# Performance work log

Hardware: AMD Instinct MI355X
Metric: run time of the kernel (lower is better)

Reference implementation:

```python
import jax, jax.numpy as jnp
import numpy as np

B, S, H, E, TOP_K = 4, 2048, 1024, 16, 4


def setup_inputs() -> dict:
    key = jax.random.key(0)
    ks = jax.random.split(key, 12)
    sc = 1.0 / np.sqrt(H)
    inp = {
        "x": jax.random.normal(ks[0], (B, S, H), dtype=jnp.float32),
        "image": jax.random.normal(ks[1], (B, S, H), dtype=jnp.float32),
        "text": jax.random.normal(ks[2], (B, S, H), dtype=jnp.float32),
        "audio": jax.random.normal(ks[3], (B, S, H), dtype=jnp.float32),
        # generalized router linear
        "Wg": jax.random.uniform(ks[4], (H, E), jnp.float32, -sc, sc),
        "bg": jax.random.uniform(ks[5], (E,), jnp.float32, -sc, sc),
        # per-modality router linears
        "Wi": jax.random.uniform(ks[6], (H, E), jnp.float32, -sc, sc),
        "bi": jax.random.uniform(ks[7], (E,), jnp.float32, -sc, sc),
        "Wt": jax.random.uniform(ks[8], (H, E), jnp.float32, -sc, sc),
        "bt": jax.random.uniform(ks[9], (E,), jnp.float32, -sc, sc),
        "Wa": jax.random.uniform(ks[10], (H, E), jnp.float32, -sc, sc),
        "ba": jax.random.uniform(ks[11], (E,), jnp.float32, -sc, sc),
    }
    return inp


def reference(x, image, text, audio, Wg, bg, Wi, bi, Wt, bt, Wa, ba):
    # combined_logits = generalized_router(x) + sum_m modality_router_m(modality_m)
    logits = (
        jnp.einsum("bsh,he->bse", x, Wg) + bg
        + jnp.einsum("bsh,he->bse", image, Wi) + bi
        + jnp.einsum("bsh,he->bse", text, Wt) + bt
        + jnp.einsum("bsh,he->bse", audio, Wa) + ba
    )  # [B,S,E]
    router_probs = jax.nn.softmax(logits, axis=-1)
    top_k_probs, top_k_indices = jax.lax.top_k(router_probs, TOP_K)
    top_k_probs = top_k_probs / jnp.sum(top_k_probs, axis=-1, keepdims=True)
    prob_per_expert = jnp.mean(router_probs, axis=(0, 1))  # [E]
    aux_loss = jnp.sum(prob_per_expert * jnp.log(prob_per_expert * E + 1e-9))
    return (top_k_indices, top_k_probs, aux_loss)
```

## Files before the change

kernel.cpp:

```cpp
#include <hip/hip_runtime.h>
#include <math.h>

constexpr int kTokens = 8192;
constexpr int kH      = 1024;
constexpr int kE      = 16;
constexpr int kTopK   = 4;
constexpr int kNC     = 16;

__global__ __launch_bounds__(256, 5)
void router_fmac(const float* __restrict__ x,   const float* __restrict__ img,
                 const float* __restrict__ txt, const float* __restrict__ aud,
                 const float* __restrict__ Wg,  const float* __restrict__ Wi,
                 const float* __restrict__ Wt,  const float* __restrict__ Wa,
                 float* __restrict__ partials)
{
    __shared__ float smem[5120];

    const int t  = threadIdx.x;
    const int w  = __builtin_amdgcn_readfirstlane(t >> 6);
    const int ln = t & 63;
    const int hs    = blockIdx.x & 15;
    const int tg    = blockIdx.x >> 4;
    const int tok0  = tg * 64;
    const int hbase = hs * 64;

    const float* Xs[4] = { x,  img, txt, aud };
    const float* Ws[4] = { Wg, Wi,  Wt,  Wa  };

    const int sc = t & 7;
    const int sr = t >> 3;

    {
        const float* src = Xs[0] + (size_t)tok0 * kH + hbase + sc * 4;
        const float4 va = *(const float4*)(src + (size_t)sr * kH);
        const float4 vb = *(const float4*)(src + (size_t)(sr + 32) * kH);
        *(float4*)&smem[sr * 36 + sc * 4] = va;
        *(float4*)&smem[(sr + 32) * 36 + sc * 4] = vb;
    }
    __syncthreads();

    double dacc[kE];
#pragma unroll
    for (int e = 0; e < kE; ++e) dacc[e] = 0.0;
    float facc[kE];

#pragma unroll
    for (int p = 0; p < 8; ++p) {
        const int m = p >> 1;
        const int s = p & 1;

        float4 na, nb;
        if (p < 7) {
            const int m2 = (p + 1) >> 1, s2 = (p + 1) & 1;
            const float* src = Xs[m2] + (size_t)tok0 * kH + hbase + s2 * 32 + sc * 4;
            na = *(const float4*)(src + (size_t)sr * kH);
            nb = *(const float4*)(src + (size_t)(sr + 32) * kH);
        }

        if (s == 0) {
#pragma unroll
            for (int e = 0; e < kE; ++e) facc[e] = 0.f;
        }

        const float* buf   = smem + (p & 1) * 2304;
        const float* wbase = Ws[m] + (size_t)(hbase + s * 32 + w * 8) * kE;

#pragma unroll
        for (int k4 = 0; k4 < 2; ++k4) {
            const float4 xv = *(const float4*)&buf[ln * 36 + w * 8 + k4 * 4];
#pragma unroll
            for (int j = 0; j < 4; ++j) {
                const float xh = (j == 0) ? xv.x : (j == 1) ? xv.y : (j == 2) ? xv.z : xv.w;
                const float* wr = wbase + (k4 * 4 + j) * kE;
                const float4 w0 = *(const float4*)(wr + 0);
                const float4 w1 = *(const float4*)(wr + 4);
                const float4 w2 = *(const float4*)(wr + 8);
                const float4 w3 = *(const float4*)(wr + 12);
                facc[0]  += xh * w0.x;  facc[1]  += xh * w0.y;
                facc[2]  += xh * w0.z;  facc[3]  += xh * w0.w;
                facc[4]  += xh * w1.x;  facc[5]  += xh * w1.y;
                facc[6]  += xh * w1.z;  facc[7]  += xh * w1.w;
                facc[8]  += xh * w2.x;  facc[9]  += xh * w2.y;
                facc[10] += xh * w2.z;  facc[11] += xh * w2.w;
                facc[12] += xh * w3.x;  facc[13] += xh * w3.y;
                facc[14] += xh * w3.z;  facc[15] += xh * w3.w;
            }
        }

        if (s == 1) {
#pragma unroll
            for (int e = 0; e < kE; ++e) dacc[e] += (double)facc[e];
        }

        if (p < 7) {
            float* nbuf = smem + ((p + 1) & 1) * 2304;
            *(float4*)&nbuf[sr * 36 + sc * 4] = na;
            *(float4*)&nbuf[(sr + 32) * 36 + sc * 4] = nb;
        }
        __syncthreads();
    }

#pragma unroll
    for (int q = 0; q < 4; ++q) {
        *(float4*)&smem[(w * 64 + ln) * 20 + q * 4] =
            make_float4((float)dacc[q * 4 + 0], (float)dacc[q * 4 + 1],
                        (float)dacc[q * 4 + 2], (float)dacc[q * 4 + 3]);
    }
    __syncthreads();
    {
        const int tok = t >> 2;
        const int eq  = t & 3;
        double s0 = 0.0, s1 = 0.0, s2 = 0.0, s3 = 0.0;
#pragma unroll
        for (int ww = 0; ww < 4; ++ww) {
            const float4 v = *(const float4*)&smem[(ww * 64 + tok) * 20 + eq * 4];
            s0 += (double)v.x;  s1 += (double)v.y;
            s2 += (double)v.z;  s3 += (double)v.w;
        }
        *(float4*)&partials[((size_t)hs * kTokens + tok0 + tok) * kE + eq * 4] =
            make_float4((float)s0, (float)s1, (float)s2, (float)s3);
    }
}

__global__ __launch_bounds__(256)
void router_topk(const float* __restrict__ partials,
                 const float* __restrict__ bg, const float* __restrict__ bi,
                 const float* __restrict__ bt, const float* __restrict__ ba,
                 float* __restrict__ out, float* __restrict__ blocksum)
{
    __shared__ double lgs[64][kE + 1];
    __shared__ float  pr[64][kE + 1];

    const int t    = threadIdx.x;
    const int tq   = t >> 2;
    const int eq   = t & 3;
    const int tok0 = blockIdx.x * 64;

    double a0 = (double)bg[eq*4+0] + (double)bi[eq*4+0] + (double)bt[eq*4+0] + (double)ba[eq*4+0];
    double a1 = (double)bg[eq*4+1] + (double)bi[eq*4+1] + (double)bt[eq*4+1] + (double)ba[eq*4+1];
    double a2 = (double)bg[eq*4+2] + (double)bi[eq*4+2] + (double)bt[eq*4+2] + (double)ba[eq*4+2];
    double a3 = (double)bg[eq*4+3] + (double)bi[eq*4+3] + (double)bt[eq*4+3] + (double)ba[eq*4+3];

#pragma unroll
    for (int c = 0; c < kNC; ++c) {
        const float4 v = *(const float4*)(partials + ((size_t)c * kTokens + tok0 + tq) * kE + eq * 4);
        a0 += (double)v.x;  a1 += (double)v.y;  a2 += (double)v.z;  a3 += (double)v.w;
    }
    lgs[tq][eq*4+0] = a0;  lgs[tq][eq*4+1] = a1;
    lgs[tq][eq*4+2] = a2;  lgs[tq][eq*4+3] = a3;
    __syncthreads();

    if (t < 64) {
        const int tok = tok0 + t;
        double lg[kE];
#pragma unroll
        for (int e = 0; e < kE; ++e) lg[e] = lgs[t][e];

        double mx = lg[0];
#pragma unroll
        for (int e = 1; e < kE; ++e) mx = fmax(mx, lg[e]);

        float p[kE];
        float sum = 0.f;
#pragma unroll
        for (int e = 0; e < kE; ++e) {
            p[e] = expf((float)(lg[e] - mx));
            sum += p[e];
        }
        const float inv = 1.f / sum;
#pragma unroll
        for (int e = 0; e < kE; ++e) { p[e] *= inv; pr[t][e] = p[e]; }

        unsigned used = 0;
        float tp[kTopK];
        int   ti[kTopK];
        float s4 = 0.f;
#pragma unroll
        for (int k = 0; k < kTopK; ++k) {
            float best = -1.f;
            int   bidx = 0;
#pragma unroll
            for (int e = 0; e < kE; ++e) {
                if (!((used >> e) & 1u) && p[e] > best) { best = p[e]; bidx = e; }
            }
            used |= 1u << bidx;
            tp[k] = best;
            ti[k] = bidx;
            s4 += best;
        }
        const float rn = 1.f / s4;

        *(float4*)&out[(size_t)tok * kTopK] =
            make_float4((float)ti[0], (float)ti[1], (float)ti[2], (float)ti[3]);
        *(float4*)&out[(size_t)kTokens * kTopK + (size_t)tok * kTopK] =
            make_float4(tp[0] * rn, tp[1] * rn, tp[2] * rn, tp[3] * rn);
    }
    __syncthreads();

    if (t < kE) {
        float s = 0.f;
#pragma unroll
        for (int tk = 0; tk < 64; ++tk) s += pr[tk][t];
        blocksum[blockIdx.x * kE + t] = s;
    }
}

__global__ __launch_bounds__(64)
void router_aux(const float* __restrict__ blocksum, float* __restrict__ out)
{
    __shared__ double ps[kE];
    const int t = threadIdx.x;
    if (t < kE) {
        double s = 0.0;
        for (int b = 0; b < 128; ++b) s += (double)blocksum[b * kE + t];
        ps[t] = s / (double)kTokens;
    }
    __syncthreads();
    if (t == 0) {
        double aux = 0.0;
#pragma unroll
        for (int e = 0; e < kE; ++e) aux += ps[e] * log(ps[e] * (double)kE + 1e-9);
        out[(size_t)kTokens * kTopK * 2] = (float)aux;
    }
}

extern "C" void kernel_launch(void* const* d_in, const int* in_sizes, int n_in,
                              void* d_out, int out_size, void* d_ws, size_t ws_size,
                              hipStream_t stream)
{
    const float* x   = (const float*)d_in[0];
    const float* img = (const float*)d_in[1];
    const float* txt = (const float*)d_in[2];
    const float* aud = (const float*)d_in[3];
    const float* Wg  = (const float*)d_in[4];
    const float* bg  = (const float*)d_in[5];
    const float* Wi  = (const float*)d_in[6];
    const float* bi  = (const float*)d_in[7];
    const float* Wt  = (const float*)d_in[8];
    const float* bt  = (const float*)d_in[9];
    const float* Wa  = (const float*)d_in[10];
    const float* ba  = (const float*)d_in[11];

    float* out      = (float*)d_out;
    float* partials = (float*)d_ws;
    float* blocksum = (float*)((char*)d_ws + (size_t)kNC * kTokens * kE * 4);

    router_fmac<<<2048, 256, 0, stream>>>(x, img, txt, aud, Wg, Wi, Wt, Wa, partials);
    router_topk<<<128, 256, 0, stream>>>(partials, bg, bi, bt, ba, out, blocksum);
    router_aux<<<1, 64, 0, stream>>>(blocksum, out);
}
```

Before: 181.9 us.

## Widen H slice per block to 128 and halve split-K partials; parallelize aux reduction

The GEMV kernel now gives each block a 128-wide H slice instead of 64, so each wave processes 16 H columns per stage. This halves the number of split-K partial buffers (16 to 8), cutting partial-sum writes and reads in the top-k kernel, and halves the block count. Each stage now loads four float4 rows per thread with a 68-float padded LDS row. The aux reduction is also spread over 128 threads. The trade-off is more LDS per block, occupancy lowered from 5 to 4 blocks, and fewer blocks to hide memory latency.

```diff
diff --git a/kernel.cpp b/kernel.cpp
--- a/kernel.cpp
+++ b/kernel.cpp
@@ -5,73 +5,78 @@
 constexpr int kH      = 1024;
 constexpr int kE      = 16;
 constexpr int kTopK   = 4;
-constexpr int kNC     = 16;
-
-__global__ __launch_bounds__(256, 5)
+constexpr int kNC     = 8;
+
+__global__ __launch_bounds__(256, 4)
 void router_fmac(const float* __restrict__ x,   const float* __restrict__ img,
                  const float* __restrict__ txt, const float* __restrict__ aud,
                  const float* __restrict__ Wg,  const float* __restrict__ Wi,
                  const float* __restrict__ Wt,  const float* __restrict__ Wa,
                  float* __restrict__ partials)
 {
-    __shared__ float smem[5120];
+    __shared__ float smem[2 * 64 * 68];
 
     const int t  = threadIdx.x;
     const int w  = __builtin_amdgcn_readfirstlane(t >> 6);
     const int ln = t & 63;
-    const int hs    = blockIdx.x & 15;
-    const int tg    = blockIdx.x >> 4;
+    const int hs    = blockIdx.x & 7;
+    const int tg    = blockIdx.x >> 3;
     const int tok0  = tg * 64;
-    const int hbase = hs * 64;
+    const int hbase = hs * 128;
 
     const float* Xs[4] = { x,  img, txt, aud };
     const float* Ws[4] = { Wg, Wi,  Wt,  Wa  };
 
-    const int sc = t & 7;
-    const int sr = t >> 3;
+    const int sc = t & 15;
+    const int sr = t >> 4;
 
     {
-        const float* src = Xs[0] + (size_t)tok0 * kH + hbase + sc * 4;
-        const float4 va = *(const float4*)(src + (size_t)sr * kH);
-        const float4 vb = *(const float4*)(src + (size_t)(sr + 32) * kH);
-        *(float4*)&smem[sr * 36 + sc * 4] = va;
-        *(float4*)&smem[(sr + 32) * 36 + sc * 4] = vb;
+        const float* src = Xs[0] + (size_t)(tok0 + sr) * kH + hbase + sc * 4;
+        const float4 v0 = *(const float4*)(src);
+        const float4 v1 = *(const float4*)(src + (size_t)16 * kH);
+        const float4 v2 = *(const float4*)(src + (size_t)32 * kH);
+        const float4 v3 = *(const float4*)(src + (size_t)48 * kH);
+        float* d = smem + sr * 68 + sc * 4;
+        *(float4*)(d)           = v0;
+        *(float4*)(d + 16 * 68) = v1;
+        *(float4*)(d + 32 * 68) = v2;
+        *(float4*)(d + 48 * 68) = v3;
     }
     __syncthreads();
 
     double dacc[kE];
 #pragma unroll
     for (int e = 0; e < kE; ++e) dacc[e] = 0.0;
-    float facc[kE];
 
 #pragma unroll
     for (int p = 0; p < 8; ++p) {
         const int m = p >> 1;
         const int s = p & 1;
 
-        float4 na, nb;
+        float4 n0, n1, n2, n3;
         if (p < 7) {
             const int m2 = (p + 1) >> 1, s2 = (p + 1) & 1;
-            const float* src = Xs[m2] + (size_t)tok0 * kH + hbase + s2 * 32 + sc * 4;
-            na = *(const float4*)(src + (size_t)sr * kH);
-            nb = *(const float4*)(src + (size_t)(sr + 32) * kH);
-        }
-
-        if (s == 0) {
-#pragma unroll
-            for (int e = 0; e < kE; ++e) facc[e] = 0.f;
-        }
-
-        const float* buf   = smem + (p & 1) * 2304;
-        const float* wbase = Ws[m] + (size_t)(hbase + s * 32 + w * 8) * kE;
-
-#pragma unroll
-        for (int k4 = 0; k4 < 2; ++k4) {
-            const float4 xv = *(const float4*)&buf[ln * 36 + w * 8 + k4 * 4];
+            const float* src = Xs[m2] + (size_t)(tok0 + sr) * kH + hbase + s2 * 64 + sc * 4;
+            n0 = *(const float4*)(src);
+            n1 = *(const float4*)(src + (size_t)16 * kH);
+            n2 = *(const float4*)(src + (size_t)32 * kH);
+            n3 = *(const float4*)(src + (size_t)48 * kH);
+        }
+
+        float facc[kE];
+#pragma unroll
+        for (int e = 0; e < kE; ++e) facc[e] = 0.f;
+
+        const float* buf = smem + (p & 1) * 4352 + ln * 68 + w * 16;
+        const float* wb  = Ws[m] + (size_t)(hbase + s * 64 + w * 16) * kE;
+
+#pragma unroll
+        for (int k4 = 0; k4 < 4; ++k4) {
+            const float4 xv = *(const float4*)(buf + k4 * 4);
 #pragma unroll
             for (int j = 0; j < 4; ++j) {
                 const float xh = (j == 0) ? xv.x : (j == 1) ? xv.y : (j == 2) ? xv.z : xv.w;
-                const float* wr = wbase + (k4 * 4 + j) * kE;
+                const float* wr = wb + (k4 * 4 + j) * kE;
                 const float4 w0 = *(const float4*)(wr + 0);
                 const float4 w1 = *(const float4*)(wr + 4);
                 const float4 w2 = *(const float4*)(wr + 8);
@@ -87,15 +92,15 @@
             }
         }
 
-        if (s == 1) {
-#pragma unroll
-            for (int e = 0; e < kE; ++e) dacc[e] += (double)facc[e];
-        }
+#pragma unroll
+        for (int e = 0; e < kE; ++e) dacc[e] += (double)facc[e];
 
         if (p < 7) {
-            float* nbuf = smem + ((p + 1) & 1) * 2304;
-            *(float4*)&nbuf[sr * 36 + sc * 4] = na;
-            *(float4*)&nbuf[(sr + 32) * 36 + sc * 4] = nb;
+            float* nbuf = smem + ((p + 1) & 1) * 4352 + sr * 68 + sc * 4;
+            *(float4*)(nbuf)           = n0;
+            *(float4*)(nbuf + 16 * 68) = n1;
+            *(float4*)(nbuf + 32 * 68) = n2;
+            *(float4*)(nbuf + 48 * 68) = n3;
         }
         __syncthreads();
     }
@@ -205,21 +210,33 @@
     }
 }
 
-__global__ __launch_bounds__(64)
+__global__ __launch_bounds__(256)
 void router_aux(const float* __restrict__ blocksum, float* __restrict__ out)
 {
-    __shared__ double ps[kE];
+    __shared__ double ps[8][kE];
+    __shared__ double fin[kE];
     const int t = threadIdx.x;
+    if (t < 128) {
+        const int e  = t & 15;
+        const int bq = t >> 4;
+        double s = 0.0;
+#pragma unroll
+        for (int k = 0; k < 16; ++k)
+            s += (double)blocksum[(bq * 16 + k) * kE + e];
+        ps[bq][e] = s;
+    }
+    __syncthreads();
     if (t < kE) {
         double s = 0.0;
-        for (int b = 0; b < 128; ++b) s += (double)blocksum[b * kE + t];
-        ps[t] = s / (double)kTokens;
+#pragma unroll
+        for (int q = 0; q < 8; ++q) s += ps[q][t];
+        fin[t] = s / (double)kTokens;
     }
     __syncthreads();
     if (t == 0) {
         double aux = 0.0;
 #pragma unroll
-        for (int e = 0; e < kE; ++e) aux += ps[e] * log(ps[e] * (double)kE + 1e-9);
+        for (int e = 0; e < kE; ++e) aux += fin[e] * log(fin[e] * (double)kE + 1e-9);
         out[(size_t)kTokens * kTopK * 2] = (float)aux;
     }
 }
@@ -245,7 +262,7 @@
     float* partials = (float*)d_ws;
     float* blocksum = (float*)((char*)d_ws + (size_t)kNC * kTokens * kE * 4);
 
-    router_fmac<<<2048, 256, 0, stream>>>(x, img, txt, aud, Wg, Wi, Wt, Wa, partials);
+    router_fmac<<<1024, 256, 0, stream>>>(x, img, txt, aud, Wg, Wi, Wt, Wa, partials);
     router_topk<<<128, 256, 0, stream>>>(partials, bg, bi, bt, ba, out, blocksum);
-    router_aux<<<1, 64, 0, stream>>>(blocksum, out);
-}
+    router_aux<<<1, 256, 0, stream>>>(blocksum, out);
+}
```

Result: slower. 194.0 us (+6.7%).

## Use per-wave private LDS buffers in router GEMM and widen top-k/aux parallelism

Applied to the files above, without the earlier changes.

The main kernel now stages into wave-private LDS tiles: each wave loads exactly the H columns it consumes. Block-wide __syncthreads in the 8-phase loop become s_waitcnt plus a scheduling barrier, which also shrinks the LDS footprint. The top-k kernel moves to 32 tokens per block over twice as many blocks, with the 16 partial chunks split across thread pairs. The aux kernel reduces block sums with 256 threads. This removes block barriers and spreads the tail work, but it relies on the lgkmcnt wait alone to order LDS accesses within a wave. The aux kernel now reads 256 block sums, matching the doubled top-k grid.

```diff
diff --git a/kernel.cpp b/kernel.cpp
--- a/kernel.cpp
+++ b/kernel.cpp
@@ -14,7 +14,7 @@
                  const float* __restrict__ Wt,  const float* __restrict__ Wa,
                  float* __restrict__ partials)
 {
-    __shared__ float smem[5120];
+    __shared__ float smem[2 * 4 * 64 * 12];
 
     const int t  = threadIdx.x;
     const int w  = __builtin_amdgcn_readfirstlane(t >> 6);
@@ -27,17 +27,21 @@
     const float* Xs[4] = { x,  img, txt, aud };
     const float* Ws[4] = { Wg, Wi,  Wt,  Wa  };
 
-    const int sc = t & 7;
-    const int sr = t >> 3;
+    const int c2 = ln & 1;
+    const int rA = ln >> 1;
+
+    float* wbuf0 = smem + w * 768;
+    float* wbuf1 = smem + 3072 + w * 768;
 
     {
-        const float* src = Xs[0] + (size_t)tok0 * kH + hbase + sc * 4;
-        const float4 va = *(const float4*)(src + (size_t)sr * kH);
-        const float4 vb = *(const float4*)(src + (size_t)(sr + 32) * kH);
-        *(float4*)&smem[sr * 36 + sc * 4] = va;
-        *(float4*)&smem[(sr + 32) * 36 + sc * 4] = vb;
-    }
-    __syncthreads();
+        const float* src = Xs[0] + (size_t)(tok0 + rA) * kH + hbase + w * 8 + c2 * 4;
+        const float4 va = *(const float4*)(src);
+        const float4 vb = *(const float4*)(src + (size_t)32 * kH);
+        *(float4*)&wbuf0[rA * 12 + c2 * 4]        = va;
+        *(float4*)&wbuf0[(rA + 32) * 12 + c2 * 4] = vb;
+    }
+    asm volatile("s_waitcnt lgkmcnt(0)" ::: "memory");
+    __builtin_amdgcn_sched_barrier(0);
 
     double dacc[kE];
 #pragma unroll
@@ -52,9 +56,9 @@
         float4 na, nb;
         if (p < 7) {
             const int m2 = (p + 1) >> 1, s2 = (p + 1) & 1;
-            const float* src = Xs[m2] + (size_t)tok0 * kH + hbase + s2 * 32 + sc * 4;
-            na = *(const float4*)(src + (size_t)sr * kH);
-            nb = *(const float4*)(src + (size_t)(sr + 32) * kH);
+            const float* src = Xs[m2] + (size_t)(tok0 + rA) * kH + hbase + s2 * 32 + w * 8 + c2 * 4;
+            na = *(const float4*)(src);
+            nb = *(const float4*)(src + (size_t)32 * kH);
         }
 
         if (s == 0) {
@@ -62,12 +66,12 @@
             for (int e = 0; e < kE; ++e) facc[e] = 0.f;
         }
 
-        const float* buf   = smem + (p & 1) * 2304;
+        const float* buf   = (p & 1) ? wbuf1 : wbuf0;
         const float* wbase = Ws[m] + (size_t)(hbase + s * 32 + w * 8) * kE;
 
 #pragma unroll
         for (int k4 = 0; k4 < 2; ++k4) {
-            const float4 xv = *(const float4*)&buf[ln * 36 + w * 8 + k4 * 4];
+            const float4 xv = *(const float4*)&buf[ln * 12 + k4 * 4];
 #pragma unroll
             for (int j = 0; j < 4; ++j) {
                 const float xh = (j == 0) ? xv.x : (j == 1) ? xv.y : (j == 2) ? xv.z : xv.w;
@@ -93,13 +97,15 @@
         }
 
         if (p < 7) {
-            float* nbuf = smem + ((p + 1) & 1) * 2304;
-            *(float4*)&nbuf[sr * 36 + sc * 4] = na;
-            *(float4*)&nbuf[(sr + 32) * 36 + sc * 4] = nb;
-        }
-        __syncthreads();
-    }
-
+            float* nbuf = (p & 1) ? wbuf0 : wbuf1;
+            *(float4*)&nbuf[rA * 12 + c2 * 4]        = na;
+            *(float4*)&nbuf[(rA + 32) * 12 + c2 * 4] = nb;
+        }
+        asm volatile("s_waitcnt lgkmcnt(0)" ::: "memory");
+        __builtin_amdgcn_sched_barrier(0);
+    }
+
+    __syncthreads();
 #pragma unroll
     for (int q = 0; q < 4; ++q) {
         *(float4*)&smem[(w * 64 + ln) * 20 + q * 4] =
@@ -128,33 +134,38 @@
                  const float* __restrict__ bt, const float* __restrict__ ba,
                  float* __restrict__ out, float* __restrict__ blocksum)
 {
-    __shared__ double lgs[64][kE + 1];
-    __shared__ float  pr[64][kE + 1];
+    __shared__ double lgs[32][2][kE + 2];
+    __shared__ float  pr[32][kE + 1];
 
     const int t    = threadIdx.x;
-    const int tq   = t >> 2;
-    const int eq   = t & 3;
-    const int tok0 = blockIdx.x * 64;
-
-    double a0 = (double)bg[eq*4+0] + (double)bi[eq*4+0] + (double)bt[eq*4+0] + (double)ba[eq*4+0];
-    double a1 = (double)bg[eq*4+1] + (double)bi[eq*4+1] + (double)bt[eq*4+1] + (double)ba[eq*4+1];
-    double a2 = (double)bg[eq*4+2] + (double)bi[eq*4+2] + (double)bt[eq*4+2] + (double)ba[eq*4+2];
-    double a3 = (double)bg[eq*4+3] + (double)bi[eq*4+3] + (double)bt[eq*4+3] + (double)ba[eq*4+3];
-
-#pragma unroll
-    for (int c = 0; c < kNC; ++c) {
+    const int tq   = t >> 3;
+    const int eq   = (t >> 1) & 3;
+    const int hc   = t & 1;
+    const int tok0 = blockIdx.x * 32;
+
+    double a0 = 0.0, a1 = 0.0, a2 = 0.0, a3 = 0.0;
+    if (hc == 0) {
+        a0 = (double)bg[eq*4+0] + (double)bi[eq*4+0] + (double)bt[eq*4+0] + (double)ba[eq*4+0];
+        a1 = (double)bg[eq*4+1] + (double)bi[eq*4+1] + (double)bt[eq*4+1] + (double)ba[eq*4+1];
+        a2 = (double)bg[eq*4+2] + (double)bi[eq*4+2] + (double)bt[eq*4+2] + (double)ba[eq*4+2];
+        a3 = (double)bg[eq*4+3] + (double)bi[eq*4+3] + (double)bt[eq*4+3] + (double)ba[eq*4+3];
+    }
+
+#pragma unroll
+    for (int c8 = 0; c8 < 8; ++c8) {
+        const int c = hc * 8 + c8;
         const float4 v = *(const float4*)(partials + ((size_t)c * kTokens + tok0 + tq) * kE + eq * 4);
         a0 += (double)v.x;  a1 += (double)v.y;  a2 += (double)v.z;  a3 += (double)v.w;
     }
-    lgs[tq][eq*4+0] = a0;  lgs[tq][eq*4+1] = a1;
-    lgs[tq][eq*4+2] = a2;  lgs[tq][eq*4+3] = a3;
-    __syncthreads();
-
-    if (t < 64) {
+    lgs[tq][hc][eq*4+0] = a0;  lgs[tq][hc][eq*4+1] = a1;
+    lgs[tq][hc][eq*4+2] = a2;  lgs[tq][hc][eq*4+3] = a3;
+    __syncthreads();
+
+    if (t < 32) {
         const int tok = tok0 + t;
         double lg[kE];
 #pragma unroll
-        for (int e = 0; e < kE; ++e) lg[e] = lgs[t][e];
+        for (int e = 0; e < kE; ++e) lg[e] = lgs[t][0][e] + lgs[t][1][e];
 
         double mx = lg[0];
 #pragma unroll
@@ -200,26 +211,38 @@
     if (t < kE) {
         float s = 0.f;
 #pragma unroll
-        for (int tk = 0; tk < 64; ++tk) s += pr[tk][t];
+        for (int tk = 0; tk < 32; ++tk) s += pr[tk][t];
         blocksum[blockIdx.x * kE + t] = s;
     }
 }
 
-__global__ __launch_bounds__(64)
+__global__ __launch_bounds__(256)
 void router_aux(const float* __restrict__ blocksum, float* __restrict__ out)
 {
-    __shared__ double ps[kE];
+    __shared__ double ps[16][kE];
+    __shared__ double fin[kE];
     const int t = threadIdx.x;
+    {
+        const int e  = t & 15;
+        const int bq = t >> 4;
+        double s = 0.0;
+#pragma unroll
+        for (int k = 0; k < 16; ++k)
+            s += (double)blocksum[(bq * 16 + k) * kE + e];
+        ps[bq][e] = s;
+    }
+    __syncthreads();
     if (t < kE) {
         double s = 0.0;
-        for (int b = 0; b < 128; ++b) s += (double)blocksum[b * kE + t];
-        ps[t] = s / (double)kTokens;
+#pragma unroll
+        for (int q = 0; q < 16; ++q) s += ps[q][t];
+        fin[t] = s / (double)kTokens;
     }
     __syncthreads();
     if (t == 0) {
         double aux = 0.0;
 #pragma unroll
-        for (int e = 0; e < kE; ++e) aux += ps[e] * log(ps[e] * (double)kE + 1e-9);
+        for (int e = 0; e < kE; ++e) aux += fin[e] * log(fin[e] * (double)kE + 1e-9);
         out[(size_t)kTokens * kTopK * 2] = (float)aux;
     }
 }
@@ -246,6 +269,6 @@
     float* blocksum = (float*)((char*)d_ws + (size_t)kNC * kTokens * kE * 4);
 
     router_fmac<<<2048, 256, 0, stream>>>(x, img, txt, aud, Wg, Wi, Wt, Wa, partials);
-    router_topk<<<128, 256, 0, stream>>>(partials, bg, bi, bt, ba, out, blocksum);
-    router_aux<<<1, 64, 0, stream>>>(blocksum, out);
-}
+    router_topk<<<256, 256, 0, stream>>>(partials, bg, bi, bt, ba, out, blocksum);
+    router_aux<<<1, 256, 0, stream>>>(blocksum, out);
+}
```

New measurement: 187.4 us. +3.1%, slower.
